# Kernel tuning notes

Hardware: AMD Instinct MI355X
Metric: run time of the kernel (lower is better)

## Reference

```python
import jax, jax.numpy as jnp
import numpy as np

EMBED_DIM = 512
NUM_HEADS = 8
HEAD_DIM = EMBED_DIM // NUM_HEADS
REL_MAX = 16
NUM_POS_IDS = 2 * REL_MAX + 1 + 1  # 34 (directed + padding id)
PADDING_IDX = 0
B, S = 2, 2048


def setup_inputs() -> dict:
    key = jax.random.key(0)
    ks = jax.random.split(key, 9)
    Q = jax.random.normal(ks[0], (B, S, EMBED_DIM), dtype=jnp.float32)
    K = jax.random.normal(ks[1], (B, S, EMBED_DIM), dtype=jnp.float32)
    V = jax.random.normal(ks[2], (B, S, EMBED_DIM), dtype=jnp.float32)
    rel_pos_ids = jax.random.randint(ks[3], (B, S, S), 0, NUM_POS_IDS, dtype=jnp.int64) if jax.config.jax_enable_x64 else jax.random.randint(ks[3], (B, S, S), 0, NUM_POS_IDS, dtype=jnp.int32)
    scale = 0.02
    Wq = jax.random.normal(ks[4], (EMBED_DIM, EMBED_DIM), dtype=jnp.float32) * scale
    Wk = jax.random.normal(ks[5], (EMBED_DIM, EMBED_DIM), dtype=jnp.float32) * scale
    Wv = jax.random.normal(ks[6], (EMBED_DIM, EMBED_DIM), dtype=jnp.float32) * scale
    Wo = jax.random.normal(ks[7], (EMBED_DIM, EMBED_DIM), dtype=jnp.float32) * scale
    rel_emb = jax.random.normal(ks[8], (NUM_POS_IDS, EMBED_DIM), dtype=jnp.float32) * scale
    rel_emb = rel_emb.at[PADDING_IDX].set(0.0)  # nn.Embedding padding_idx row is zero
    return {"Q": Q, "K": K, "V": V, "rel_pos_ids": rel_pos_ids,
            "Wq": Wq, "Wk": Wk, "Wv": Wv, "Wo": Wo, "rel_emb": rel_emb}


def _proj(x, W):
    # Linear (no bias) then strided head split: view(B, S, head_dim, H) -> (B, H, S, head_dim)
    b, s, _ = x.shape
    y = x @ W.T
    return y.reshape(b, s, HEAD_DIM, NUM_HEADS).transpose(0, 3, 1, 2)


def _forward(Q, K, V, rel_pos_ids, Wq, Wk, Wv, Wo, rel_emb):
    b, sq, _ = Q.shape
    Qp = _proj(Q, Wq)  # (B, H, Sq, hd)
    Kp = _proj(K, Wk)  # (B, H, Sk, hd)
    Vp = _proj(V, Wv)  # (B, H, Sk, hd)

    # rel_embeds split per head with the same strided layout: (P, hd, H) -> (H, P, hd)
    R = rel_emb.reshape(NUM_POS_IDS, HEAD_DIM, NUM_HEADS).transpose(2, 0, 1)
    # Q_rel: (B, H, Sq, P)
    Q_rel = jnp.einsum('bhsd,hpd->bhsp', Qp, R)
    # gather per-pair relative bias: (B, H, Sq, Sk)
    rel_shift = jnp.take_along_axis(Q_rel, rel_pos_ids[:, None, :, :], axis=3)
    mask = (rel_pos_ids == PADDING_IDX)[:, None, :, :]
    rel_shift = jnp.where(mask, -jnp.inf, rel_shift)

    energy = (jnp.einsum('bhqd,bhkd->bhqk', Qp, Kp) + rel_shift) / jnp.sqrt(jnp.float32(HEAD_DIM))
    attn = jax.nn.softmax(energy, axis=-1)
    out = jnp.einsum('bhqk,bhkd->bhqd', attn, Vp)  # (B, H, Sq, hd)
    # inverse of strided split: (B, Sq, hd, H) -> flatten last two
    out = out.transpose(0, 2, 3, 1).reshape(b, sq, EMBED_DIM)
    return out @ Wo.T


def reference(Q, K, V, rel_pos_ids, Wq, Wk, Wv, Wo, rel_emb):
    return _forward(Q, K, V, rel_pos_ids, Wq, Wk, Wv, Wo, rel_emb)
```

## Files before the change

kernel.cpp:

```cpp
#include <hip/hip_runtime.h>
#include <cstdint>
#include <cstddef>

#define SEQ   2048
#define BBAT  2
#define EMBED 512
#define NH    8
#define HD    64
#define NPOS  34

typedef __bf16 bf16;
typedef __bf16 bf16x8 __attribute__((ext_vector_type(8)));
typedef float  f32x4  __attribute__((ext_vector_type(4)));

#define ESCALE 0.1803368801111204f

__device__ __forceinline__ f32x4 mfma16(bf16x8 a, bf16x8 b, f32x4 c){
  return __builtin_amdgcn_mfma_f32_16x16x32_bf16(a, b, c, 0, 0, 0);
}

__global__ __launch_bounds__(256) void k_prep(
    const float* __restrict__ Q, const float* __restrict__ K, const float* __restrict__ V,
    const float* __restrict__ Wq, const float* __restrict__ Wk,
    const float* __restrict__ Wv, const float* __restrict__ Wo,
    const float* __restrict__ RE,
    bf16* __restrict__ Qb, bf16* __restrict__ Kb, bf16* __restrict__ Vb,
    bf16* __restrict__ Wall, bf16* __restrict__ Rb)
{
  const int NCONV = 3*524288;
  const int NW = 196608, NO = 262144;
  int i = blockIdx.x*256 + threadIdx.x;
  if (i < NCONV){
    int tsel = i >> 19, j = i & 524287;
    const float* s = tsel==0 ? Q : (tsel==1 ? K : V);
    bf16* d       = tsel==0 ? Qb : (tsel==1 ? Kb : Vb);
    float4 v = ((const float4*)s)[j];
    union { bf16 e[4]; ushort4 u; } pk;
    pk.e[0]=(bf16)v.x; pk.e[1]=(bf16)v.y; pk.e[2]=(bf16)v.z; pk.e[3]=(bf16)v.w;
    ((ushort4*)d)[j] = pk.u;
  } else {
    int j = i - NCONV;
    if (j < NW){
      int w  = j >> 16;
      int r  = j & 65535;
      int np = r >> 7, c4 = (r & 127) << 2;
      const float* W = (w==0) ? Wq : ((w==1) ? Wk : Wv);
      int src = ((np & 63) << 3) + (np >> 6);
      float4 v = *(const float4*)(W + (size_t)src*512 + c4);
      union { bf16 e[4]; ushort4 u; } pk;
      pk.e[0]=(bf16)v.x; pk.e[1]=(bf16)v.y; pk.e[2]=(bf16)v.z; pk.e[3]=(bf16)v.w;
      *(ushort4*)(Wall + (size_t)w*262144 + (size_t)np*512 + c4) = pk.u;
    } else if (j < NW + NO){
      int jj = j - NW;
      int n = jj >> 9, kp = jj & 511;
      int src = ((kp & 63) << 3) + (kp >> 6);
      Wall[(size_t)3*262144 + (size_t)n*512 + kp] = (bf16)Wo[(size_t)n*512 + src];
    } else {
      int jj = j - NW - NO;
      if (jj < 8*48*64){
        int h  = jj / (48*64);
        int r2 = jj - h*(48*64);
        int p  = r2 >> 6, dd = r2 & 63;
        float v = (p < NPOS) ? RE[(size_t)p*512 + dd*8 + h] : 0.f;
        Rb[jj] = (bf16)v;
      }
    }
  }
}

__global__ __launch_bounds__(256,2) void k_gemm_proj(
    const bf16* __restrict__ Qb, const bf16* __restrict__ Kb, const bf16* __restrict__ Vb,
    const bf16* __restrict__ W,  bf16* __restrict__ Qp, bf16* __restrict__ Kp, bf16* __restrict__ Vt)
{
  const bf16* A  = blockIdx.z==0 ? Qb : (blockIdx.z==1 ? Kb : Vb);
  const bf16* Bw = W + (size_t)blockIdx.z*262144;

  __shared__ __align__(16) bf16 As[128][72];
  __shared__ __align__(16) bf16 Bs[64][72];
  const int t = threadIdx.x;
  const int w = t >> 6, lane = t & 63, l15 = lane & 15, quad = lane >> 4;
  const int wm = (w & 1) * 64, wn = (w >> 1) * 32;
  const int m0 = blockIdx.y * 128, n0 = blockIdx.x * 64;

  f32x4 acc[4][2];
  #pragma unroll
  for (int mt=0; mt<4; ++mt)
    #pragma unroll
    for (int nt=0; nt<2; ++nt) acc[mt][nt] = (f32x4){0.f,0.f,0.f,0.f};

  for (int kt = 0; kt < 512; kt += 64){
    #pragma unroll
    for (int i = 0; i < 4; ++i){
      int lin = t + 256*i;
      int r = lin >> 3, c8 = (lin & 7) << 3;
      *(uint4*)&As[r][c8] = *(const uint4*)(A + (size_t)(m0 + r)*512 + kt + c8);
    }
    #pragma unroll
    for (int i = 0; i < 2; ++i){
      int lin = t + 256*i;
      int r = lin >> 3, c8 = (lin & 7) << 3;
      *(uint4*)&Bs[r][c8] = *(const uint4*)(Bw + (size_t)(n0 + r)*512 + kt + c8);
    }
    __syncthreads();
    #pragma unroll
    for (int ks = 0; ks < 2; ++ks){
      bf16x8 am[4], bn[2];
      #pragma unroll
      for (int x=0;x<4;++x) am[x] = *(const bf16x8*)&As[wm + x*16 + l15][ks*32 + quad*8];
      #pragma unroll
      for (int y=0;y<2;++y) bn[y] = *(const bf16x8*)&Bs[wn + y*16 + l15][ks*32 + quad*8];
      #pragma unroll
      for (int mt=0;mt<4;++mt)
        #pragma unroll
        for (int nt=0;nt<2;++nt)
          acc[mt][nt] = mfma16(am[mt], bn[nt], acc[mt][nt]);
    }
    __syncthreads();
  }

  if (blockIdx.z != 2){
    bf16* C = blockIdx.z==0 ? Qp : Kp;
    #pragma unroll
    for (int mt=0;mt<4;++mt)
      #pragma unroll
      for (int r=0;r<4;++r){
        int m = m0 + wm + mt*16 + quad*4 + r;
        #pragma unroll
        for (int nt=0;nt<2;++nt)
          C[(size_t)m*512 + n0 + wn + nt*16 + l15] = (bf16)acc[mt][nt][r];
      }
  } else {
    bf16 (*VT)[136] = (bf16(*)[136])As;
    #pragma unroll
    for (int mt=0;mt<4;++mt)
      #pragma unroll
      for (int r=0;r<4;++r){
        int m = wm + mt*16 + quad*4 + r;
        #pragma unroll
        for (int nt=0;nt<2;++nt)
          VT[wn + nt*16 + l15][m] = (bf16)acc[mt][nt][r];
      }
    __syncthreads();
    const int h = blockIdx.x, b = m0 >> 11, s0 = m0 & 2047;
    const int n = t >> 2, c0 = (t & 3) * 32;
    bf16* dst = Vt + ((size_t)((b*NH + h)*HD + n))*SEQ + s0 + c0;
    #pragma unroll
    for (int i = 0; i < 4; ++i)
      *(uint4*)(dst + i*8) = *(const uint4*)&VT[n][c0 + i*8];
  }
}

__global__ __launch_bounds__(256,2) void k_gemm_out(
    const bf16* __restrict__ A, const bf16* __restrict__ Bw, float* __restrict__ C)
{
  __shared__ __align__(16) bf16 As[64][72];
  __shared__ __align__(16) bf16 Bs[64][72];
  const int t = threadIdx.x;
  const int w = t >> 6, lane = t & 63, l15 = lane & 15, quad = lane >> 4;
  const int wm = (w & 1) * 32, wn = (w >> 1) * 32;
  const int m0 = blockIdx.y * 64, n0 = blockIdx.x * 64;

  f32x4 acc[2][2];
  #pragma unroll
  for (int mt=0; mt<2; ++mt)
    #pragma unroll
    for (int nt=0; nt<2; ++nt) acc[mt][nt] = (f32x4){0.f,0.f,0.f,0.f};

  for (int kt = 0; kt < 512; kt += 64){
    #pragma unroll
    for (int i = 0; i < 2; ++i){
      int lin = t + 256*i;
      int r = lin >> 3, c8 = (lin & 7) << 3;
      *(uint4*)&As[r][c8] = *(const uint4*)(A  + (size_t)(m0 + r)*512 + kt + c8);
      *(uint4*)&Bs[r][c8] = *(const uint4*)(Bw + (size_t)(n0 + r)*512 + kt + c8);
    }
    __syncthreads();
    #pragma unroll
    for (int ks = 0; ks < 2; ++ks){
      bf16x8 am[2], bn[2];
      #pragma unroll
      for (int x=0;x<2;++x) am[x] = *(const bf16x8*)&As[wm + x*16 + l15][ks*32 + quad*8];
      #pragma unroll
      for (int y=0;y<2;++y) bn[y] = *(const bf16x8*)&Bs[wn + y*16 + l15][ks*32 + quad*8];
      #pragma unroll
      for (int mt=0;mt<2;++mt)
        #pragma unroll
        for (int nt=0;nt<2;++nt)
          acc[mt][nt] = mfma16(am[mt], bn[nt], acc[mt][nt]);
    }
    __syncthreads();
  }
  #pragma unroll
  for (int mt=0;mt<2;++mt)
    #pragma unroll
    for (int r=0;r<4;++r){
      int m = m0 + wm + mt*16 + quad*4 + r;
      #pragma unroll
      for (int nt=0;nt<2;++nt)
        C[(size_t)m*512 + n0 + wn + nt*16 + l15] = acc[mt][nt][r];
    }
}

__global__ __launch_bounds__(256,2) void k_attn(
    const bf16* __restrict__ Qp, const bf16* __restrict__ Kp,
    const bf16* __restrict__ Vt, const bf16* __restrict__ Rb,
    const int* __restrict__ ids, bf16* __restrict__ Out)
{
  __shared__ __align__(16) bf16 Ks[128][72];
  __shared__ __align__(16) bf16 Vs[64][136];
  __shared__ __align__(16) bf16 Ps[64][136];
  __shared__ float lut[64][35];
  __shared__ float lsum_s[128];

  const int t = threadIdx.x;
  const int b = blockIdx.z, h = blockIdx.y;
  const int q0 = blockIdx.x * 64;
  const int w = t >> 6, lane = t & 63, l15 = lane & 15, quad = lane >> 4;
  const int qh = w & 1, kh = w >> 1;

  const size_t idb = (size_t)b*SEQ*SEQ;

  int nid[2][4][4];
  #pragma unroll
  for (int mt=0; mt<2; ++mt)
    #pragma unroll
    for (int nt=0; nt<4; ++nt)
      #pragma unroll
      for (int r=0; r<4; ++r)
        nid[mt][nt][r] = ids[idb + (size_t)(q0 + qh*32 + mt*16 + quad*4 + r)*SEQ
                             + kh*64 + nt*16 + l15];

  {
    const bf16* qbrow = Qp + (size_t)(b*SEQ + q0 + w*16 + l15)*EMBED + h*HD;
    bf16x8 ab0 = *(const bf16x8*)(qbrow + quad*8);
    bf16x8 ab1 = *(const bf16x8*)(qbrow + 32 + quad*8);
    const bf16* rh = Rb + h*3072;
    #pragma unroll
    for (int nt = 0; nt < 3; ++nt){
      bf16x8 r0 = *(const bf16x8*)(rh + (nt*16 + l15)*64 + quad*8);
      bf16x8 r1 = *(const bf16x8*)(rh + (nt*16 + l15)*64 + 32 + quad*8);
      f32x4 c = (f32x4){0.f,0.f,0.f,0.f};
      c = mfma16(ab0, r0, c);
      c = mfma16(ab1, r1, c);
      int p = nt*16 + l15;
      if (p < NPOS){
        #pragma unroll
        for (int r = 0; r < 4; ++r)
          lut[w*16 + quad*4 + r][p] = (p == 0) ? 0.f : exp2f(c[r]*ESCALE);
      }
    }
  }

  bf16x8 aq[2][2];
  #pragma unroll
  for (int mt = 0; mt < 2; ++mt){
    const bf16* qrow = Qp + (size_t)(b*SEQ + q0 + qh*32 + mt*16 + l15)*EMBED + h*HD;
    aq[mt][0] = *(const bf16x8*)(qrow + quad*8);
    aq[mt][1] = *(const bf16x8*)(qrow + 32 + quad*8);
  }

  const bf16* kbase = Kp + (size_t)b*SEQ*EMBED + h*HD;
  const bf16* vbase = Vt + (size_t)(b*NH + h)*HD*SEQ;

  f32x4 acc[2][2];
  #pragma unroll
  for (int mt=0;mt<2;++mt)
    #pragma unroll
    for (int nt=0;nt<2;++nt) acc[mt][nt] = (f32x4){0.f,0.f,0.f,0.f};
  float lsum[2][4] = {{0.f,0.f,0.f,0.f},{0.f,0.f,0.f,0.f}};

  for (int kt = 0; kt < 16; ++kt){
    const int k0 = kt * 128;
    #pragma unroll
    for (int i = 0; i < 4; ++i){
      int lin = t + 256*i;
      int r = lin >> 3, c8 = (lin & 7) << 3;
      *(uint4*)&Ks[r][c8] = *(const uint4*)(kbase + (size_t)(k0 + r)*EMBED + c8);
    }
    #pragma unroll
    for (int i = 0; i < 4; ++i){
      int lin = t + 256*i;
      int d = lin >> 4, c8 = (lin & 15) << 3;
      *(uint4*)&Vs[d][c8] = *(const uint4*)(vbase + (size_t)d*SEQ + k0 + c8);
    }
    __syncthreads();

    float wv[2][4][4];
    #pragma unroll
    for (int mt = 0; mt < 2; ++mt)
      #pragma unroll
      for (int nt = 0; nt < 4; ++nt)
        #pragma unroll
        for (int r = 0; r < 4; ++r)
          wv[mt][nt][r] = lut[qh*32 + mt*16 + quad*4 + r][nid[mt][nt][r]];

    if (kt < 15){
      #pragma unroll
      for (int mt = 0; mt < 2; ++mt)
        #pragma unroll
        for (int nt = 0; nt < 4; ++nt)
          #pragma unroll
          for (int r = 0; r < 4; ++r)
            nid[mt][nt][r] = ids[idb + (size_t)(q0 + qh*32 + mt*16 + quad*4 + r)*SEQ
                                 + (k0 + 128) + kh*64 + nt*16 + l15];
    }

    f32x4 sf[2][4];
    #pragma unroll
    for (int nt = 0; nt < 4; ++nt){
      bf16x8 bk0 = *(const bf16x8*)&Ks[kh*64 + nt*16 + l15][quad*8];
      bf16x8 bk1 = *(const bf16x8*)&Ks[kh*64 + nt*16 + l15][32 + quad*8];
      #pragma unroll
      for (int mt = 0; mt < 2; ++mt){
        f32x4 c = (f32x4){0.f,0.f,0.f,0.f};
        c = mfma16(aq[mt][0], bk0, c);
        c = mfma16(aq[mt][1], bk1, c);
        sf[mt][nt] = c;
      }
    }

    #pragma unroll
    for (int mt = 0; mt < 2; ++mt)
      #pragma unroll
      for (int nt = 0; nt < 4; ++nt)
        #pragma unroll
        for (int r = 0; r < 4; ++r){
          float p = exp2f(sf[mt][nt][r]*ESCALE) * wv[mt][nt][r];
          lsum[mt][r] += p;
          Ps[qh*32 + mt*16 + quad*4 + r][kh*64 + nt*16 + l15] = (bf16)p;
        }
    __syncthreads();

    #pragma unroll
    for (int kk = 0; kk < 4; ++kk){
      bf16x8 ap[2];
      #pragma unroll
      for (int mt = 0; mt < 2; ++mt)
        ap[mt] = *(const bf16x8*)&Ps[qh*32 + mt*16 + l15][kk*32 + quad*8];
      #pragma unroll
      for (int nt = 0; nt < 2; ++nt){
        bf16x8 bv = *(const bf16x8*)&Vs[kh*32 + nt*16 + l15][kk*32 + quad*8];
        #pragma unroll
        for (int mt = 0; mt < 2; ++mt)
          acc[mt][nt] = mfma16(ap[mt], bv, acc[mt][nt]);
      }
    }
    __syncthreads();
  }

  #pragma unroll
  for (int mt = 0; mt < 2; ++mt)
    #pragma unroll
    for (int r = 0; r < 4; ++r){
      float v = lsum[mt][r];
      v += __shfl_xor(v, 1); v += __shfl_xor(v, 2);
      v += __shfl_xor(v, 4); v += __shfl_xor(v, 8);
      if (l15 == 0) lsum_s[kh*64 + qh*32 + mt*16 + quad*4 + r] = v;
    }
  __syncthreads();

  #pragma unroll
  for (int mt = 0; mt < 2; ++mt){
    #pragma unroll
    for (int r = 0; r < 4; ++r){
      int ql = qh*32 + mt*16 + quad*4 + r;
      float inv = 1.f / (lsum_s[ql] + lsum_s[64 + ql]);
      #pragma unroll
      for (int nt = 0; nt < 2; ++nt){
        int d = kh*32 + nt*16 + l15;
        Out[(size_t)(b*SEQ + q0 + ql)*EMBED + h*HD + d] = (bf16)(acc[mt][nt][r]*inv);
      }
    }
  }
}

extern "C" void kernel_launch(void* const* d_in, const int* in_sizes, int n_in,
                              void* d_out, int out_size, void* d_ws, size_t ws_size,
                              hipStream_t stream)
{
  (void)in_sizes; (void)n_in; (void)out_size;
  const float* Q  = (const float*)d_in[0];
  const float* K  = (const float*)d_in[1];
  const float* V  = (const float*)d_in[2];
  const int*   ID = (const int*)d_in[3];
  const float* Wq = (const float*)d_in[4];
  const float* Wk = (const float*)d_in[5];
  const float* Wv = (const float*)d_in[6];
  const float* Wo = (const float*)d_in[7];
  const float* RE = (const float*)d_in[8];
  float* out = (float*)d_out;

  const size_t MB = (size_t)1 << 20;
  if (ws_size < 36*MB) return;
  char* ws = (char*)d_ws;
  bf16*  Qb    = (bf16*)(ws + 0*MB);
  bf16*  Kb    = (bf16*)(ws + 4*MB);
  bf16*  Vb    = (bf16*)(ws + 8*MB);
  bf16*  Qp    = (bf16*)(ws + 12*MB);
  bf16*  Kp    = (bf16*)(ws + 16*MB);
  bf16*  Vt    = (bf16*)(ws + 20*MB);
  bf16*  Wall  = (bf16*)(ws + 24*MB);
  bf16*  Wop   = Wall + (size_t)3*262144;
  bf16*  Rb    = (bf16*)(ws + 26*MB);
  bf16*  AO    = (bf16*)(ws + 0*MB);

  k_prep      <<<dim3(8032),    256, 0, stream>>>(Q, K, V, Wq, Wk, Wv, Wo, RE,
                                                  Qb, Kb, Vb, Wall, Rb);
  k_gemm_proj <<<dim3(8,32,3),  256, 0, stream>>>(Qb, Kb, Vb, Wall, Qp, Kp, Vt);
  k_attn      <<<dim3(32,8,2),  256, 0, stream>>>(Qp, Kp, Vt, Rb, ID, AO);
  k_gemm_out  <<<dim3(8,64),    256, 0, stream>>>(AO, Wop, out);
}
```

Baseline: 192.7 us.

## Transpose QK^T MFMA, fold scale into Q, vectorize id loads and packed P stores

Folds the softmax scale into Q during projection and stores raw relative-bias logits in the LUT, so the bias is added before one exp2 instead of multiplying two exponentials. The QK^T MFMA swaps operands so each lane holds four consecutive keys of one query row. This turns rel_pos_ids loads into 16-byte vector loads, P stores into packed 8-byte writes, and the row-sum into a two-step shuffle. It also adds s_setprio around the MFMA blocks and uses the hardware rcp and exp2 intrinsics. Padding now relies on exp2 of -1e30 underflowing to zero, and the scaled Q is rounded to bf16, which changes precision slightly.

```diff
diff --git a/kernel.cpp b/kernel.cpp
--- a/kernel.cpp
+++ b/kernel.cpp
@@ -12,6 +12,7 @@
 typedef __bf16 bf16;
 typedef __bf16 bf16x8 __attribute__((ext_vector_type(8)));
 typedef float  f32x4  __attribute__((ext_vector_type(4)));
+typedef int    int32x4 __attribute__((ext_vector_type(4)));
 
 #define ESCALE 0.1803368801111204f
 
@@ -120,6 +121,7 @@
 
   if (blockIdx.z != 2){
     bf16* C = blockIdx.z==0 ? Qp : Kp;
+    const float scl = (blockIdx.z==0) ? ESCALE : 1.0f;
     #pragma unroll
     for (int mt=0;mt<4;++mt)
       #pragma unroll
@@ -127,7 +129,7 @@
         int m = m0 + wm + mt*16 + quad*4 + r;
         #pragma unroll
         for (int nt=0;nt<2;++nt)
-          C[(size_t)m*512 + n0 + wn + nt*16 + l15] = (bf16)acc[mt][nt][r];
+          C[(size_t)m*512 + n0 + wn + nt*16 + l15] = (bf16)(acc[mt][nt][r] * scl);
       }
   } else {
     bf16 (*VT)[136] = (bf16(*)[136])As;
@@ -220,15 +222,14 @@
 
   const size_t idb = (size_t)b*SEQ*SEQ;
 
-  int nid[2][4][4];
+  int32x4 nid[2][4];
   #pragma unroll
   for (int mt=0; mt<2; ++mt)
     #pragma unroll
     for (int nt=0; nt<4; ++nt)
-      #pragma unroll
-      for (int r=0; r<4; ++r)
-        nid[mt][nt][r] = ids[idb + (size_t)(q0 + qh*32 + mt*16 + quad*4 + r)*SEQ
-                             + kh*64 + nt*16 + l15];
+      nid[mt][nt] = *(const int32x4*)(ids + idb
+          + (size_t)(q0 + qh*32 + mt*16 + l15)*SEQ
+          + kh*64 + nt*16 + quad*4);
 
   {
     const bf16* qbrow = Qp + (size_t)(b*SEQ + q0 + w*16 + l15)*EMBED + h*HD;
@@ -246,17 +247,17 @@
       if (p < NPOS){
         #pragma unroll
         for (int r = 0; r < 4; ++r)
-          lut[w*16 + quad*4 + r][p] = (p == 0) ? 0.f : exp2f(c[r]*ESCALE);
-      }
-    }
-  }
-
-  bf16x8 aq[2][2];
+          lut[w*16 + quad*4 + r][p] = (p == 0) ? -1e30f : c[r];
+      }
+    }
+  }
+
+  bf16x8 bq[2][2];
   #pragma unroll
   for (int mt = 0; mt < 2; ++mt){
     const bf16* qrow = Qp + (size_t)(b*SEQ + q0 + qh*32 + mt*16 + l15)*EMBED + h*HD;
-    aq[mt][0] = *(const bf16x8*)(qrow + quad*8);
-    aq[mt][1] = *(const bf16x8*)(qrow + 32 + quad*8);
+    bq[mt][0] = *(const bf16x8*)(qrow + quad*8);
+    bq[mt][1] = *(const bf16x8*)(qrow + 32 + quad*8);
   }
 
   const bf16* kbase = Kp + (size_t)b*SEQ*EMBED + h*HD;
@@ -267,7 +268,7 @@
   for (int mt=0;mt<2;++mt)
     #pragma unroll
     for (int nt=0;nt<2;++nt) acc[mt][nt] = (f32x4){0.f,0.f,0.f,0.f};
-  float lsum[2][4] = {{0.f,0.f,0.f,0.f},{0.f,0.f,0.f,0.f}};
+  float lsum[2] = {0.f, 0.f};
 
   for (int kt = 0; kt < 16; ++kt){
     const int k0 = kt * 128;
@@ -287,50 +288,62 @@
 
     float wv[2][4][4];
     #pragma unroll
-    for (int mt = 0; mt < 2; ++mt)
-      #pragma unroll
-      for (int nt = 0; nt < 4; ++nt)
-        #pragma unroll
-        for (int r = 0; r < 4; ++r)
-          wv[mt][nt][r] = lut[qh*32 + mt*16 + quad*4 + r][nid[mt][nt][r]];
+    for (int mt = 0; mt < 2; ++mt){
+      const float* lr = &lut[qh*32 + mt*16 + l15][0];
+      #pragma unroll
+      for (int nt = 0; nt < 4; ++nt){
+        int32x4 v = nid[mt][nt];
+        wv[mt][nt][0] = lr[v[0]];
+        wv[mt][nt][1] = lr[v[1]];
+        wv[mt][nt][2] = lr[v[2]];
+        wv[mt][nt][3] = lr[v[3]];
+      }
+    }
 
     if (kt < 15){
       #pragma unroll
       for (int mt = 0; mt < 2; ++mt)
         #pragma unroll
         for (int nt = 0; nt < 4; ++nt)
-          #pragma unroll
-          for (int r = 0; r < 4; ++r)
-            nid[mt][nt][r] = ids[idb + (size_t)(q0 + qh*32 + mt*16 + quad*4 + r)*SEQ
-                                 + (k0 + 128) + kh*64 + nt*16 + l15];
+          nid[mt][nt] = *(const int32x4*)(ids + idb
+              + (size_t)(q0 + qh*32 + mt*16 + l15)*SEQ
+              + (k0 + 128) + kh*64 + nt*16 + quad*4);
     }
 
     f32x4 sf[2][4];
+    __builtin_amdgcn_s_setprio(1);
     #pragma unroll
     for (int nt = 0; nt < 4; ++nt){
-      bf16x8 bk0 = *(const bf16x8*)&Ks[kh*64 + nt*16 + l15][quad*8];
-      bf16x8 bk1 = *(const bf16x8*)&Ks[kh*64 + nt*16 + l15][32 + quad*8];
+      bf16x8 ak0 = *(const bf16x8*)&Ks[kh*64 + nt*16 + l15][quad*8];
+      bf16x8 ak1 = *(const bf16x8*)&Ks[kh*64 + nt*16 + l15][32 + quad*8];
       #pragma unroll
       for (int mt = 0; mt < 2; ++mt){
         f32x4 c = (f32x4){0.f,0.f,0.f,0.f};
-        c = mfma16(aq[mt][0], bk0, c);
-        c = mfma16(aq[mt][1], bk1, c);
+        c = mfma16(ak0, bq[mt][0], c);
+        c = mfma16(ak1, bq[mt][1], c);
         sf[mt][nt] = c;
       }
     }
-
-    #pragma unroll
-    for (int mt = 0; mt < 2; ++mt)
-      #pragma unroll
-      for (int nt = 0; nt < 4; ++nt)
-        #pragma unroll
-        for (int r = 0; r < 4; ++r){
-          float p = exp2f(sf[mt][nt][r]*ESCALE) * wv[mt][nt][r];
-          lsum[mt][r] += p;
-          Ps[qh*32 + mt*16 + quad*4 + r][kh*64 + nt*16 + l15] = (bf16)p;
-        }
-    __syncthreads();
-
+    __builtin_amdgcn_s_setprio(0);
+
+    #pragma unroll
+    for (int mt = 0; mt < 2; ++mt){
+      #pragma unroll
+      for (int nt = 0; nt < 4; ++nt){
+        union { bf16 e[4]; uint2 u; } pk;
+        float p0 = __builtin_amdgcn_exp2f(sf[mt][nt][0] + wv[mt][nt][0]);
+        float p1 = __builtin_amdgcn_exp2f(sf[mt][nt][1] + wv[mt][nt][1]);
+        float p2 = __builtin_amdgcn_exp2f(sf[mt][nt][2] + wv[mt][nt][2]);
+        float p3 = __builtin_amdgcn_exp2f(sf[mt][nt][3] + wv[mt][nt][3]);
+        pk.e[0] = (bf16)p0; pk.e[1] = (bf16)p1;
+        pk.e[2] = (bf16)p2; pk.e[3] = (bf16)p3;
+        lsum[mt] += (p0 + p1) + (p2 + p3);
+        *(uint2*)&Ps[qh*32 + mt*16 + l15][kh*64 + nt*16 + quad*4] = pk.u;
+      }
+    }
+    __syncthreads();
+
+    __builtin_amdgcn_s_setprio(1);
     #pragma unroll
     for (int kk = 0; kk < 4; ++kk){
       bf16x8 ap[2];
@@ -345,18 +358,17 @@
           acc[mt][nt] = mfma16(ap[mt], bv, acc[mt][nt]);
       }
     }
-    __syncthreads();
-  }
-
-  #pragma unroll
-  for (int mt = 0; mt < 2; ++mt)
-    #pragma unroll
-    for (int r = 0; r < 4; ++r){
-      float v = lsum[mt][r];
-      v += __shfl_xor(v, 1); v += __shfl_xor(v, 2);
-      v += __shfl_xor(v, 4); v += __shfl_xor(v, 8);
-      if (l15 == 0) lsum_s[kh*64 + qh*32 + mt*16 + quad*4 + r] = v;
-    }
+    __builtin_amdgcn_s_setprio(0);
+    __syncthreads();
+  }
+
+  #pragma unroll
+  for (int mt = 0; mt < 2; ++mt){
+    float v = lsum[mt];
+    v += __shfl_xor(v, 16);
+    v += __shfl_xor(v, 32);
+    if (quad == 0) lsum_s[kh*64 + qh*32 + mt*16 + l15] = v;
+  }
   __syncthreads();
 
   #pragma unroll
@@ -364,7 +376,7 @@
     #pragma unroll
     for (int r = 0; r < 4; ++r){
       int ql = qh*32 + mt*16 + quad*4 + r;
-      float inv = 1.f / (lsum_s[ql] + lsum_s[64 + ql]);
+      float inv = __builtin_amdgcn_rcpf(lsum_s[ql] + lsum_s[64 + ql]);
       #pragma unroll
       for (int nt = 0; nt < 2; ++nt){
         int d = kh*32 + nt*16 + l15;
```

Result: no change. 190.6 us (-1.1%).
